# Kernel tuning notes

Hardware: AMD Instinct MI355X
Metric: run time of the kernel (lower is better)

The kernel has to match this reference:

```python
import jax, jax.numpy as jnp
import numpy as np

B, T, C = 4, 1024, 512      # batch, seq_len, n_attn
H, TT, D = 1, 1024, 16      # n_head (forced to 1 by kv.view), ctx_len, head_size


def setup_inputs() -> dict:
    key = jax.random.key(0)
    ks = jax.random.split(key, 13)
    s = 0.02
    return {
        "x": jax.random.normal(ks[0], (B, T, C), jnp.float32),
        "time_w": 1.0 + 0.1 * jax.random.normal(ks[1], (H, TT), jnp.float32),
        "time_alpha": 1.0 + 0.1 * jax.random.normal(ks[2], (H, 1, TT), jnp.float32),
        "time_beta": 1.0 + 0.1 * jax.random.normal(ks[3], (H, TT, 1), jnp.float32),
        "time_gamma": 1.0 + 0.1 * jax.random.normal(ks[4], (TT, 1), jnp.float32),
        "Wk": s * jax.random.normal(ks[5], (D, C), jnp.float32),
        "bk": jnp.zeros((D,), jnp.float32),
        "Wv": s * jax.random.normal(ks[6], (D, C), jnp.float32),
        "bv": jnp.zeros((D,), jnp.float32),
        "Wr": s * jax.random.normal(ks[7], (D, C), jnp.float32),
        "br": jnp.zeros((D,), jnp.float32),
        "Wo": s * jax.random.normal(ks[8], (64, D), jnp.float32),
        "bo": jnp.zeros((64,), jnp.float32),
    }


def reference(x, time_w, time_alpha, time_beta, time_gamma,
              Wk, bk, Wv, bv, Wr, br, Wo, bo):
    Tq = x.shape[1]
    # --- Toeplitz decay-matrix build (pad / tile / reshape trick) ---
    w = jnp.pad(time_w, ((0, 0), (0, TT)))                    # [H, 2TT]
    w = jnp.tile(w, (1, TT))[:, :-TT]                         # [H, 2TT*TT - TT]
    w = w.reshape(-1, TT, 2 * TT - 1)[:, :, TT - 1:]          # [H, TT, TT]
    w = w[:, :Tq, :Tq] * time_alpha[:, :, :Tq] * time_beta[:, :Tq, :]  # [H, T, T]
    # --- time shift on first half of channels (ZeroPad2d((0,0,1,-1))) ---
    half = x.shape[-1] // 2
    xs = jnp.pad(x[:, :, :half], ((0, 0), (1, 0), (0, 0)))[:, :-1]   # shift right by 1
    xx = jnp.concatenate([xs, x[:, :, half:]], axis=-1)              # [B, T, C]
    # --- k / v / r projections ---
    k = jnp.exp(jnp.clip(xx @ Wk.T + bk, -60.0, 30.0))        # [B, T, D]
    v = xx @ Wv.T + bv                                        # [B, T, D]
    r = xx @ Wr.T + br                                        # [B, T, D]
    sum_k = jnp.cumsum(k, axis=1)                             # [B, T, D]
    kv = k * v                                                # [B, T, D]
    # torch: kv.view(B,T,1,D).transpose(1,2) -> [B,1,T,D]; einsum 'htu,bthd->bhud'
    # broadcasts w's h=1 against kv's time axis and kv's t=1 against w's t axis:
    #   wkv[b,h,u,d] = (sum_t w[0,t,u]) * kv[b,h(time),d]
    w_sum = jnp.sum(w, axis=1)[0]                             # [T] over u
    wkv_full = w_sum[None, None, :, None] * kv[:, :, None, :] # [B, T, T, D]
    wkv = jnp.mean(wkv_full, axis=1)                          # mean over h -> [B, T, D]
    rwkv = r * wkv / (sum_k + 1e-8)                           # [B, T, D]
    out = (rwkv @ Wo.T + bo) * time_gamma[:Tq, :]             # [B, T, 64]
    return out
```

## Files before the change

kernel.cpp:

```cpp
#include <hip/hip_runtime.h>
#include <hip/hip_bf16.h>

typedef __hip_bfloat16 bf16;


__device__ __forceinline__ float ldf(const void* p, int f, long idx) {
    if (f == 0) return ((const float*)p)[idx];
    if (f == 1) {
        unsigned int u = ((unsigned int)((const unsigned short*)p)[idx]) << 16;
        float r; __builtin_memcpy(&r, &u, 4); return r;
    }
    return 0.f;
}

__device__ __forceinline__ float4 ld4(const void* p, int f, long idx) {
    if (f == 0) return ((const float4*)p)[idx >> 2];
    if (f == 1) {
        const unsigned short* sp = (const unsigned short*)p + idx;
        unsigned int u0 = ((unsigned int)sp[0]) << 16;
        unsigned int u1 = ((unsigned int)sp[1]) << 16;
        unsigned int u2 = ((unsigned int)sp[2]) << 16;
        unsigned int u3 = ((unsigned int)sp[3]) << 16;
        float4 r;
        __builtin_memcpy(&r.x, &u0, 4); __builtin_memcpy(&r.y, &u1, 4);
        __builtin_memcpy(&r.z, &u2, 4); __builtin_memcpy(&r.w, &u3, 4);
        return r;
    }
    return make_float4(0.f, 0.f, 0.f, 0.f);
}

__device__ __forceinline__ void sniff13(const void* const* ps, const int* ns,
                                        int tid, unsigned* mall, int* sf) {
    unsigned m = 0;
    for (int t = tid; t < 13 * 64; t += 256) {
        int p = t >> 6, j = t & 63;
        int n16 = ns[p] < 64 ? ns[p] : 64;
        if (j < n16) {
            unsigned short v = ((const unsigned short*)ps[p])[j];
            if (v != 0) m |= (1u << p);
        }
    }
    for (int t = tid; t < 13 * 32; t += 256) {
        int p = t >> 5, jp = t & 31;
        int n16 = ns[p] < 64 ? ns[p] : 64; int npair = n16 >> 1;
        if (jp < npair) {
            const unsigned short* u = (const unsigned short*)ps[p];
            unsigned short lo = u[2 * jp], hi = u[2 * jp + 1];
            int elo = (lo >> 7) & 0xFF, ehi = (hi >> 7) & 0xFF;
            bool lo_ok = (elo >= 64 && elo <= 190) || lo == 0;
            bool hi_ok = (ehi >= 64 && ehi <= 190) || hi == 0;
            if (!(lo_ok && hi_ok)) m |= (1u << (16 + p));
        }
    }
    #pragma unroll
    for (int off = 1; off < 64; off <<= 1) m |= __shfl_xor(m, off);
    if (tid == 0) *mall = 0;
    __syncthreads();
    if ((tid & 63) == 0) atomicOr(mall, m);
    __syncthreads();
    unsigned mm = *mall;
    if (tid < 13) {
        int f;
        if (!((mm >> tid) & 1)) f = 2;
        else f = ((mm >> (16 + tid)) & 1) ? 0 : 1;
        sf[tid] = f;
    }
    __syncthreads();
}

__device__ __forceinline__ float ldbias(const void* bk, const void* bv,
                                        const void* br, const int* sf, int o2) {
    if (o2 < 16) return ldf(bk, sf[6], o2);
    if (o2 < 32) return ldf(bv, sf[8], o2 - 16);
    if (o2 < 48) return ldf(br, sf[10], o2 - 32);
    return 0.f;
}

__global__ __launch_bounds__(256) void proj_kernel(
    const void* x, const void* tw, const void* alpha, const void* beta,
    const void* gamma, const void* Wk, const void* bk, const void* Wv,
    const void* bv, const void* Wr, const void* br, const void* Wo,
    const void* bo,
    int n0, int n1, int n2, int n3, int n4, int n5, int n6, int n7,
    int n8, int n9, int n10, int n11, int n12,
    float* __restrict__ k_ws, float* __restrict__ r_ws,
    float* __restrict__ blkS, float* __restrict__ blkKV,
    float* __restrict__ w_sum, int* __restrict__ flags)
{
    __shared__ float xs[8 * 512];
    __shared__ float sred[8][48];
    __shared__ float kred[128], kvred[128];
    __shared__ float wsred[4];
    __shared__ int sf[16];
    __shared__ unsigned mall;
    int tid = threadIdx.x;
    const void* ps[13] = {x,tw,alpha,beta,gamma,Wk,bk,Wv,bv,Wr,br,Wo,bo};
    int ns[13] = {n0,n1,n2,n3,n4,n5,n6,n7,n8,n9,n10,n11,n12};
    sniff13(ps, ns, tid, &mall, sf);

    if (blockIdx.x == 0 && tid < 14) {
        if (tid == 13) {
            int any16 = 0;
            for (int j = 0; j < 13; ++j) if (sf[j] == 1) any16 = 1;
            flags[13] = any16;
        } else {
            flags[tid] = sf[tid];
        }
    }

    int row0 = blockIdx.x * 8;
    int b = row0 >> 10;
    int lt0 = row0 & 1023;
    int fx = sf[0];

    if (fx == 1) {
        const unsigned short* xp = (const unsigned short*)x;
        #pragma unroll
        for (int j = 0; j < 4; ++j) {
            int v = tid + 256 * j;
            int el = v * 4;
            int r = el >> 9, c = el & 511;
            int lt = lt0 + r - ((c < 256) ? 1 : 0);
            float4 f;
            if (lt < 0) f = make_float4(0.f, 0.f, 0.f, 0.f);
            else {
                const unsigned short* sp = xp + ((long)(b * 1024 + lt) * 512 + c);
                unsigned int u0 = ((unsigned int)sp[0]) << 16;
                unsigned int u1 = ((unsigned int)sp[1]) << 16;
                unsigned int u2 = ((unsigned int)sp[2]) << 16;
                unsigned int u3 = ((unsigned int)sp[3]) << 16;
                __builtin_memcpy(&f.x, &u0, 4); __builtin_memcpy(&f.y, &u1, 4);
                __builtin_memcpy(&f.z, &u2, 4); __builtin_memcpy(&f.w, &u3, 4);
            }
            reinterpret_cast<float4*>(xs)[v] = f;
        }
    } else {
        const float* xp = (const float*)x;
        #pragma unroll
        for (int j = 0; j < 4; ++j) {
            int v = tid + 256 * j;
            int el = v * 4;
            int r = el >> 9, c = el & 511;
            int lt = lt0 + r - ((c < 256) ? 1 : 0);
            float4 f;
            if (lt < 0) f = make_float4(0.f, 0.f, 0.f, 0.f);
            else f = *reinterpret_cast<const float4*>(xp + ((long)(b * 1024 + lt) * 512 + c));
            reinterpret_cast<float4*>(xs)[v] = f;
        }
    }
    __syncthreads();

    int lane = tid & 63, wv = tid >> 6;
    const float4* xs4 = reinterpret_cast<const float4*>(xs);
    const void* Wm[3] = {Wk, Wv, Wr};
    int fwm[3] = {sf[5], sf[7], sf[9]};
    #pragma unroll
    for (int m = 0; m < 3; ++m) {
        const void* Wp = Wm[m]; int fw = fwm[m];
        float acc[4][8];
        #pragma unroll
        for (int oi = 0; oi < 4; ++oi)
            #pragma unroll
            for (int r = 0; r < 8; ++r) acc[oi][r] = 0.f;

        if (fw == 0) {
            const float4* Wq = reinterpret_cast<const float4*>(Wp);
            #pragma unroll
            for (int j = 0; j < 2; ++j) {
                int c4 = lane + 64 * j;
                float4 xr[8];
                #pragma unroll
                for (int r = 0; r < 8; ++r) xr[r] = xs4[r * 128 + c4];
                #pragma unroll
                for (int oi = 0; oi < 4; ++oi) {
                    int row = wv * 4 + oi;
                    float4 wq = Wq[row * 128 + c4];
                    #pragma unroll
                    for (int r = 0; r < 8; ++r)
                        acc[oi][r] += xr[r].x * wq.x + xr[r].y * wq.y +
                                      xr[r].z * wq.z + xr[r].w * wq.w;
                }
            }
        } else {
            #pragma unroll
            for (int j = 0; j < 2; ++j) {
                int c4 = lane + 64 * j;
                float4 xr[8];
                #pragma unroll
                for (int r = 0; r < 8; ++r) xr[r] = xs4[r * 128 + c4];
                #pragma unroll
                for (int oi = 0; oi < 4; ++oi) {
                    int row = wv * 4 + oi;
                    float4 wq = ld4(Wp, fw, (long)row * 512 + c4 * 4);
                    #pragma unroll
                    for (int r = 0; r < 8; ++r)
                        acc[oi][r] += xr[r].x * wq.x + xr[r].y * wq.y +
                                      xr[r].z * wq.z + xr[r].w * wq.w;
                }
            }
        }
        #pragma unroll
        for (int oi = 0; oi < 4; ++oi) {
            #pragma unroll
            for (int r = 0; r < 8; ++r) {
                float a = acc[oi][r];
                a += __shfl_xor(a, 1);  a += __shfl_xor(a, 2);
                a += __shfl_xor(a, 4);  a += __shfl_xor(a, 8);
                a += __shfl_xor(a, 16); a += __shfl_xor(a, 32);
                if (lane == oi * 8 + r)
                    sred[r][m * 16 + wv * 4 + oi] = a;
            }
        }
    }
    __syncthreads();

    #pragma unroll
    for (int it = 0; it < 2; ++it) {
        int idx = tid + 256 * it;
        int o2 = idx & 63, r2 = idx >> 6;
        if (o2 < 48) {
            float s = ldbias(bk, bv, br, sf, o2) + sred[r2][o2];
            long a = (long)(lt0 + r2) * 64 + b * 16 + (o2 & 15);
            if (o2 < 16) {
                k_ws[a] = expf(fminf(fmaxf(s, -60.f), 30.f));
            } else if (o2 < 32) {
                int d = o2 - 16;
                float sk = ldbias(bk, bv, br, sf, d) + sred[r2][d];
                float kk = expf(fminf(fmaxf(sk, -60.f), 30.f));
                kred[d * 8 + r2] = kk;
                kvred[d * 8 + r2] = kk * s;
            } else {
                r_ws[a] = s;
            }
        }
    }
    __syncthreads();
    if (tid < 16) {
        float sk = 0.f, skv = 0.f;
        #pragma unroll
        for (int r = 0; r < 8; ++r) { sk += kred[tid * 8 + r]; skv += kvred[tid * 8 + r]; }
        blkS[(long)blockIdx.x * 16 + tid] = sk;
        blkKV[(long)blockIdx.x * 16 + tid] = skv;
    }

    {
        int g = tid >> 7, l = tid & 127;
        int u = blockIdx.x * 2 + g;
        int n = 1024 - u;
        int ftw = sf[1], fbe = sf[3];
        float acc = 0.f;
        for (int s = l; s < n; s += 128)
            acc += ldf(tw, ftw, 1023 - s) * ldf(beta, fbe, u + s);
        #pragma unroll
        for (int off = 32; off > 0; off >>= 1) acc += __shfl_xor(acc, off);
        if ((tid & 63) == 0) wsred[tid >> 6] = acc;
        __syncthreads();
        if ((tid & 127) == 0)
            w_sum[u] = (wsred[g * 2] + wsred[g * 2 + 1]) * ldf(alpha, sf[2], u);
    }
}

__global__ __launch_bounds__(256) void out_kernel(
    const void* gamma, const void* Wo, const void* bo,
    const float* __restrict__ k_ws, const float* __restrict__ r_ws,
    const float* __restrict__ blkS, const float* __restrict__ blkKV,
    const float* __restrict__ w_sum, const int* __restrict__ flags,
    void* __restrict__ out)
{
    __shared__ float redc[256], redk[256];
    __shared__ float cums[16], kvm[16], kk8[8][16], rr8[8][16], rw[8][16];
    __shared__ int sfl[16];
    int tid = threadIdx.x;
    if (tid < 16) sfl[tid] = flags[tid];

    int row0 = blockIdx.x * 8;
    int b = row0 >> 10;
    int t0 = row0 & 1023;
    int nch = t0 >> 3;
    long base = (long)b * 16;

    {
        int d = tid & 15, lane = tid >> 4;
        float pc = 0.f, pk = 0.f;
        for (int ch = lane; ch < nch; ch += 16) pc += blkS[((long)b * 128 + ch) * 16 + d];
        for (int ch = lane; ch < 128; ch += 16) pk += blkKV[((long)b * 128 + ch) * 16 + d];
        redc[tid] = pc; redk[tid] = pk;
    }
    if (tid < 128) {
        int rl = tid >> 4, dd = tid & 15;
        kk8[rl][dd] = k_ws[(long)(t0 + rl) * 64 + base + dd];
    } else {
        int tt = tid - 128; int rl = tt >> 4, dd = tt & 15;
        rr8[rl][dd] = r_ws[(long)(t0 + rl) * 64 + base + dd];
    }
    __syncthreads();
    if (tid < 16) {
        float c = 0.f, kv = 0.f;
        #pragma unroll
        for (int ln = 0; ln < 16; ++ln) { c += redc[ln * 16 + tid]; kv += redk[ln * 16 + tid]; }
        cums[tid] = c;
        kvm[tid] = kv * (1.0f / 1024.0f);
    }
    __syncthreads();

    if (tid < 128) {
        int rl = tid >> 4, o = tid & 15;
        float ck = cums[o];
        for (int i = 0; i <= rl; ++i) ck += kk8[i][o];
        rw[rl][o] = rr8[rl][o] * w_sum[t0 + rl] * kvm[o] / (ck + 1e-8f);
    }
    __syncthreads();

    int fWo = sfl[11], fbo = sfl[12], fga = sfl[4], any16 = sfl[13];
    if (fWo == 0) {
        const float4* Wq = reinterpret_cast<const float4*>(Wo);
        #pragma unroll
        for (int it = 0; it < 2; ++it) {
            int idx = tid + 256 * it;
            int rl = idx >> 6, o = idx & 63;
            int t = t0 + rl;
            float acc = ldf(bo, fbo, o);
            #pragma unroll
            for (int j = 0; j < 4; ++j) {
                float4 w = Wq[o * 4 + j];
                acc += rw[rl][4 * j + 0] * w.x + rw[rl][4 * j + 1] * w.y +
                       rw[rl][4 * j + 2] * w.z + rw[rl][4 * j + 3] * w.w;
            }
            float val = acc * ldf(gamma, fga, t);
            long oa = (long)(row0 + rl) * 64 + o;
            if (any16) ((bf16*)out)[oa] = __float2bfloat16(val);
            else       ((float*)out)[oa] = val;
        }
    } else {
        #pragma unroll
        for (int it = 0; it < 2; ++it) {
            int idx = tid + 256 * it;
            int rl = idx >> 6, o = idx & 63;
            int t = t0 + rl;
            float acc = ldf(bo, fbo, o);
            #pragma unroll
            for (int j = 0; j < 4; ++j) {
                float4 w = ld4(Wo, fWo, (long)o * 16 + 4 * j);
                acc += rw[rl][4 * j + 0] * w.x + rw[rl][4 * j + 1] * w.y +
                       rw[rl][4 * j + 2] * w.z + rw[rl][4 * j + 3] * w.w;
            }
            float val = acc * ldf(gamma, fga, t);
            long oa = (long)(row0 + rl) * 64 + o;
            if (any16) ((bf16*)out)[oa] = __float2bfloat16(val);
            else       ((float*)out)[oa] = val;
        }
    }
}

extern "C" void kernel_launch(void* const* d_in, const int* in_sizes, int n_in,
                              void* d_out, int out_size, void* d_ws, size_t ws_size,
                              hipStream_t stream) {
    const void* x     = d_in[0];
    const void* tw    = d_in[1];
    const void* alpha = d_in[2];
    const void* beta  = d_in[3];
    const void* gamma = d_in[4];
    const void* Wk    = d_in[5];
    const void* bk    = d_in[6];
    const void* Wv    = d_in[7];
    const void* bv    = d_in[8];
    const void* Wr    = d_in[9];
    const void* br    = d_in[10];
    const void* Wo    = d_in[11];
    const void* bo    = d_in[12];

    float* ws    = (float*)d_ws;
    float* k_ws  = ws;
    float* r_ws  = ws + 65536;
    float* blkS  = ws + 131072;
    float* blkKV = ws + 139264;
    float* w_sum = ws + 147456;
    int*   flags = (int*)(ws + 148480);

    proj_kernel<<<512, 256, 0, stream>>>(
        x, tw, alpha, beta, gamma, Wk, bk, Wv, bv, Wr, br, Wo, bo,
        in_sizes[0], in_sizes[1], in_sizes[2], in_sizes[3], in_sizes[4],
        in_sizes[5], in_sizes[6], in_sizes[7], in_sizes[8], in_sizes[9],
        in_sizes[10], in_sizes[11], in_sizes[12],
        k_ws, r_ws, blkS, blkKV, w_sum, flags);
    out_kernel<<<512, 256, 0, stream>>>(
        gamma, Wo, bo, k_ws, r_ws, blkS, blkKV, w_sum, flags, (void*)d_out);
}
```

Before: 115.2 us.

## Fuse projection and output kernels into one persistent kernel with grid barriers

Replaces the two-kernel pipeline with a single 1024-block kernel that uses software grid barriers: one to zero the segment accumulators and build w_sum, and one after the k/v/r projections. Per-block partial sums become atomicAdds into per-64-row segment buffers, which shortens the prefix scan in the output phase. This removes a kernel launch and the second pass over block partials, but depends on all 1024 blocks being co-resident (launch_bounds 256,4), adds a memset, and adds spin-wait costs.

Result: slower. 167.7 us (+45.6%).

```diff
diff --git a/kernel.cpp b/kernel.cpp
--- a/kernel.cpp
+++ b/kernel.cpp
@@ -29,6 +29,13 @@
     return make_float4(0.f, 0.f, 0.f, 0.f);
 }
 
+__device__ __forceinline__ void stc(float* p, float v) {
+    __hip_atomic_store(p, v, __ATOMIC_RELAXED, __HIP_MEMORY_SCOPE_AGENT);
+}
+__device__ __forceinline__ float ldc(const float* p) {
+    return __hip_atomic_load(p, __ATOMIC_RELAXED, __HIP_MEMORY_SCOPE_AGENT);
+}
+
 __device__ __forceinline__ void sniff13(const void* const* ps, const int* ns,
                                         int tid, unsigned* mall, int* sf) {
     unsigned m = 0;
@@ -68,15 +75,20 @@
     __syncthreads();
 }
 
-__device__ __forceinline__ float ldbias(const void* bk, const void* bv,
-                                        const void* br, const int* sf, int o2) {
-    if (o2 < 16) return ldf(bk, sf[6], o2);
-    if (o2 < 32) return ldf(bv, sf[8], o2 - 16);
-    if (o2 < 48) return ldf(br, sf[10], o2 - 32);
-    return 0.f;
-}
-
-__global__ __launch_bounds__(256) void proj_kernel(
+__device__ __forceinline__ void gridbar(unsigned* cnt, unsigned target, int tid) {
+    asm volatile("s_waitcnt vmcnt(0)" ::: "memory");
+    __syncthreads();
+    if (tid == 0) {
+        __hip_atomic_fetch_add(cnt, 1u, __ATOMIC_RELAXED, __HIP_MEMORY_SCOPE_AGENT);
+        while (__hip_atomic_load(cnt, __ATOMIC_RELAXED, __HIP_MEMORY_SCOPE_AGENT)
+               < target)
+            __builtin_amdgcn_s_sleep(4);
+    }
+    __syncthreads();
+    asm volatile("" ::: "memory");
+}
+
+__global__ __launch_bounds__(256, 4) void fused_kernel(
     const void* x, const void* tw, const void* alpha, const void* beta,
     const void* gamma, const void* Wk, const void* bk, const void* Wv,
     const void* bv, const void* Wr, const void* br, const void* Wo,
@@ -84,39 +96,56 @@
     int n0, int n1, int n2, int n3, int n4, int n5, int n6, int n7,
     int n8, int n9, int n10, int n11, int n12,
     float* __restrict__ k_ws, float* __restrict__ r_ws,
-    float* __restrict__ blkS, float* __restrict__ blkKV,
-    float* __restrict__ w_sum, int* __restrict__ flags)
+    float* __restrict__ w_sum, float* __restrict__ segsum,
+    float* __restrict__ segkv, unsigned* __restrict__ cnt,
+    void* __restrict__ out)
 {
-    __shared__ float xs[8 * 512];
-    __shared__ float sred[8][48];
-    __shared__ float kred[128], kvred[128];
-    __shared__ float wsred[4];
+    __shared__ float xs[4 * 512];
+    __shared__ float sred[4][48];
+    __shared__ float kred[64], kvred[64];
+    __shared__ float redc[256], redk[256];
+    __shared__ float cums[16], kvm[16], kk3[3][16], rr4[4][16], rw[4][16], wsl[4];
     __shared__ int sf[16];
     __shared__ unsigned mall;
     int tid = threadIdx.x;
     const void* ps[13] = {x,tw,alpha,beta,gamma,Wk,bk,Wv,bv,Wr,br,Wo,bo};
     int ns[13] = {n0,n1,n2,n3,n4,n5,n6,n7,n8,n9,n10,n11,n12};
+
     sniff13(ps, ns, tid, &mall, sf);
-
-    if (blockIdx.x == 0 && tid < 14) {
-        if (tid == 13) {
-            int any16 = 0;
-            for (int j = 0; j < 13; ++j) if (sf[j] == 1) any16 = 1;
-            flags[13] = any16;
-        } else {
-            flags[tid] = sf[tid];
-        }
-    }
-
-    int row0 = blockIdx.x * 8;
+    if (tid == 0) {
+        int any16 = 0;
+        for (int j = 0; j < 13; ++j) if (sf[j] == 1) any16 = 1;
+        sf[13] = any16;
+    }
+
+    int idx = blockIdx.x * 256 + tid;
+    if (idx < 1024)       stc(&segsum[idx], 0.f);
+    else if (idx < 2048)  stc(&segkv[idx - 1024], 0.f);
+
+    {
+        int u = blockIdx.x;
+        int ftw = sf[1], fal = sf[2], fbe = sf[3];
+        float acc = 0.f;
+        int n = 1024 - u;
+        for (int s = tid; s < n; s += 256)
+            acc += ldf(tw, ftw, 1023 - s) * ldf(beta, fbe, u + s);
+        redc[tid] = acc;
+        __syncthreads();
+        for (int off = 128; off > 0; off >>= 1) {
+            if (tid < off) redc[tid] += redc[tid + off];
+            __syncthreads();
+        }
+        if (tid == 0) stc(&w_sum[u], redc[0] * ldf(alpha, fal, u));
+    }
+
+    int row0 = blockIdx.x * 4;
     int b = row0 >> 10;
     int lt0 = row0 & 1023;
     int fx = sf[0];
-
     if (fx == 1) {
         const unsigned short* xp = (const unsigned short*)x;
         #pragma unroll
-        for (int j = 0; j < 4; ++j) {
+        for (int j = 0; j < 2; ++j) {
             int v = tid + 256 * j;
             int el = v * 4;
             int r = el >> 9, c = el & 511;
@@ -137,7 +166,7 @@
     } else {
         const float* xp = (const float*)x;
         #pragma unroll
-        for (int j = 0; j < 4; ++j) {
+        for (int j = 0; j < 2; ++j) {
             int v = tid + 256 * j;
             int el = v * 4;
             int r = el >> 9, c = el & 511;
@@ -148,207 +177,175 @@
             reinterpret_cast<float4*>(xs)[v] = f;
         }
     }
-    __syncthreads();
-
-    int lane = tid & 63, wv = tid >> 6;
-    const float4* xs4 = reinterpret_cast<const float4*>(xs);
-    const void* Wm[3] = {Wk, Wv, Wr};
-    int fwm[3] = {sf[5], sf[7], sf[9]};
-    #pragma unroll
-    for (int m = 0; m < 3; ++m) {
-        const void* Wp = Wm[m]; int fw = fwm[m];
-        float acc[4][8];
+
+    gridbar(cnt, 1024u, tid);
+
+    {
+        int lane = tid & 63, wv = tid >> 6;
+        const float4* xs4 = reinterpret_cast<const float4*>(xs);
+        const void* Wm[3] = {Wk, Wv, Wr};
+        int fwm[3] = {sf[5], sf[7], sf[9]};
         #pragma unroll
-        for (int oi = 0; oi < 4; ++oi)
-            #pragma unroll
-            for (int r = 0; r < 8; ++r) acc[oi][r] = 0.f;
-
-        if (fw == 0) {
-            const float4* Wq = reinterpret_cast<const float4*>(Wp);
-            #pragma unroll
-            for (int j = 0; j < 2; ++j) {
-                int c4 = lane + 64 * j;
-                float4 xr[8];
+        for (int m = 0; m < 3; ++m) {
+            const void* Wp = Wm[m]; int fw = fwm[m];
+            float acc[4][4];
+            #pragma unroll
+            for (int oi = 0; oi < 4; ++oi)
                 #pragma unroll
-                for (int r = 0; r < 8; ++r) xr[r] = xs4[r * 128 + c4];
+                for (int r = 0; r < 4; ++r) acc[oi][r] = 0.f;
+
+            if (fw == 0) {
+                const float4* Wq = reinterpret_cast<const float4*>(Wp);
                 #pragma unroll
-                for (int oi = 0; oi < 4; ++oi) {
-                    int row = wv * 4 + oi;
-                    float4 wq = Wq[row * 128 + c4];
+                for (int j = 0; j < 2; ++j) {
+                    int c4 = lane + 64 * j;
+                    float4 xr[4];
                     #pragma unroll
-                    for (int r = 0; r < 8; ++r)
-                        acc[oi][r] += xr[r].x * wq.x + xr[r].y * wq.y +
-                                      xr[r].z * wq.z + xr[r].w * wq.w;
+                    for (int r = 0; r < 4; ++r) xr[r] = xs4[r * 128 + c4];
+                    #pragma unroll
+                    for (int oi = 0; oi < 4; ++oi) {
+                        int row = wv * 4 + oi;
+                        float4 wq = Wq[row * 128 + c4];
+                        #pragma unroll
+                        for (int r = 0; r < 4; ++r)
+                            acc[oi][r] += xr[r].x * wq.x + xr[r].y * wq.y +
+                                          xr[r].z * wq.z + xr[r].w * wq.w;
+                    }
                 }
-            }
-        } else {
-            #pragma unroll
-            for (int j = 0; j < 2; ++j) {
-                int c4 = lane + 64 * j;
-                float4 xr[8];
+            } else {
                 #pragma unroll
-                for (int r = 0; r < 8; ++r) xr[r] = xs4[r * 128 + c4];
+                for (int j = 0; j < 2; ++j) {
+                    int c4 = lane + 64 * j;
+                    float4 xr[4];
+                    #pragma unroll
+                    for (int r = 0; r < 4; ++r) xr[r] = xs4[r * 128 + c4];
+                    #pragma unroll
+                    for (int oi = 0; oi < 4; ++oi) {
+                        int row = wv * 4 + oi;
+                        float4 wq = ld4(Wp, fw, (long)row * 512 + c4 * 4);
+                        #pragma unroll
+                        for (int r = 0; r < 4; ++r)
+                            acc[oi][r] += xr[r].x * wq.x + xr[r].y * wq.y +
+                                          xr[r].z * wq.z + xr[r].w * wq.w;
+                    }
+                }
+            }
+            #pragma unroll
+            for (int oi = 0; oi < 4; ++oi) {
                 #pragma unroll
-                for (int oi = 0; oi < 4; ++oi) {
-                    int row = wv * 4 + oi;
-                    float4 wq = ld4(Wp, fw, (long)row * 512 + c4 * 4);
-                    #pragma unroll
-                    for (int r = 0; r < 8; ++r)
-                        acc[oi][r] += xr[r].x * wq.x + xr[r].y * wq.y +
-                                      xr[r].z * wq.z + xr[r].w * wq.w;
+                for (int r = 0; r < 4; ++r) {
+                    float a = acc[oi][r];
+                    a += __shfl_xor(a, 1);  a += __shfl_xor(a, 2);
+                    a += __shfl_xor(a, 4);  a += __shfl_xor(a, 8);
+                    a += __shfl_xor(a, 16); a += __shfl_xor(a, 32);
+                    if (lane == oi * 4 + r)
+                        sred[r][m * 16 + wv * 4 + oi] = a;
                 }
             }
         }
-        #pragma unroll
-        for (int oi = 0; oi < 4; ++oi) {
-            #pragma unroll
-            for (int r = 0; r < 8; ++r) {
-                float a = acc[oi][r];
-                a += __shfl_xor(a, 1);  a += __shfl_xor(a, 2);
-                a += __shfl_xor(a, 4);  a += __shfl_xor(a, 8);
-                a += __shfl_xor(a, 16); a += __shfl_xor(a, 32);
-                if (lane == oi * 8 + r)
-                    sred[r][m * 16 + wv * 4 + oi] = a;
-            }
-        }
-    }
-    __syncthreads();
-
-    #pragma unroll
-    for (int it = 0; it < 2; ++it) {
-        int idx = tid + 256 * it;
-        int o2 = idx & 63, r2 = idx >> 6;
+        __syncthreads();
+
+        int o2 = tid & 63, r2 = tid >> 6;
+        int seg = lt0 >> 6;
         if (o2 < 48) {
-            float s = ldbias(bk, bv, br, sf, o2) + sred[r2][o2];
+            float s = 0.f;
+            if (o2 < 16)      s = ldf(bk, sf[6], o2);
+            else if (o2 < 32) s = ldf(bv, sf[8], o2 - 16);
+            else              s = ldf(br, sf[10], o2 - 32);
+            s += sred[r2][o2];
             long a = (long)(lt0 + r2) * 64 + b * 16 + (o2 & 15);
             if (o2 < 16) {
-                k_ws[a] = expf(fminf(fmaxf(s, -60.f), 30.f));
+                stc(&k_ws[a], expf(fminf(fmaxf(s, -60.f), 30.f)));
             } else if (o2 < 32) {
                 int d = o2 - 16;
-                float sk = ldbias(bk, bv, br, sf, d) + sred[r2][d];
+                float sk = ldf(bk, sf[6], d) + sred[r2][d];
                 float kk = expf(fminf(fmaxf(sk, -60.f), 30.f));
-                kred[d * 8 + r2] = kk;
-                kvred[d * 8 + r2] = kk * s;
+                kred[d * 4 + r2] = kk;
+                kvred[d * 4 + r2] = kk * s;
             } else {
-                r_ws[a] = s;
-            }
-        }
-    }
-    __syncthreads();
-    if (tid < 16) {
-        float sk = 0.f, skv = 0.f;
-        #pragma unroll
-        for (int r = 0; r < 8; ++r) { sk += kred[tid * 8 + r]; skv += kvred[tid * 8 + r]; }
-        blkS[(long)blockIdx.x * 16 + tid] = sk;
-        blkKV[(long)blockIdx.x * 16 + tid] = skv;
-    }
+                stc(&r_ws[a], s);
+            }
+        }
+        __syncthreads();
+        if (tid < 16) {
+            float sk = 0.f, skv = 0.f;
+            #pragma unroll
+            for (int r = 0; r < 4; ++r) { sk += kred[tid * 4 + r]; skv += kvred[tid * 4 + r]; }
+            atomicAdd(&segsum[seg * 64 + b * 16 + tid], sk);
+            atomicAdd(&segkv[seg * 64 + b * 16 + tid], skv);
+        }
+    }
+
+    gridbar(cnt, 2048u, tid);
 
     {
-        int g = tid >> 7, l = tid & 127;
-        int u = blockIdx.x * 2 + g;
-        int n = 1024 - u;
-        int ftw = sf[1], fbe = sf[3];
-        float acc = 0.f;
-        for (int s = l; s < n; s += 128)
-            acc += ldf(tw, ftw, 1023 - s) * ldf(beta, fbe, u + s);
-        #pragma unroll
-        for (int off = 32; off > 0; off >>= 1) acc += __shfl_xor(acc, off);
-        if ((tid & 63) == 0) wsred[tid >> 6] = acc;
-        __syncthreads();
-        if ((tid & 127) == 0)
-            w_sum[u] = (wsred[g * 2] + wsred[g * 2 + 1]) * ldf(alpha, sf[2], u);
-    }
-}
-
-__global__ __launch_bounds__(256) void out_kernel(
-    const void* gamma, const void* Wo, const void* bo,
-    const float* __restrict__ k_ws, const float* __restrict__ r_ws,
-    const float* __restrict__ blkS, const float* __restrict__ blkKV,
-    const float* __restrict__ w_sum, const int* __restrict__ flags,
-    void* __restrict__ out)
-{
-    __shared__ float redc[256], redk[256];
-    __shared__ float cums[16], kvm[16], kk8[8][16], rr8[8][16], rw[8][16];
-    __shared__ int sfl[16];
-    int tid = threadIdx.x;
-    if (tid < 16) sfl[tid] = flags[tid];
-
-    int row0 = blockIdx.x * 8;
-    int b = row0 >> 10;
-    int t0 = row0 & 1023;
-    int nch = t0 >> 3;
-    long base = (long)b * 16;
-
-    {
-        int d = tid & 15, lane = tid >> 4;
-        float pc = 0.f, pk = 0.f;
-        for (int ch = lane; ch < nch; ch += 16) pc += blkS[((long)b * 128 + ch) * 16 + d];
-        for (int ch = lane; ch < 128; ch += 16) pk += blkKV[((long)b * 128 + ch) * 16 + d];
-        redc[tid] = pc; redk[tid] = pk;
-    }
-    if (tid < 128) {
-        int rl = tid >> 4, dd = tid & 15;
-        kk8[rl][dd] = k_ws[(long)(t0 + rl) * 64 + base + dd];
-    } else {
-        int tt = tid - 128; int rl = tt >> 4, dd = tt & 15;
-        rr8[rl][dd] = r_ws[(long)(t0 + rl) * 64 + base + dd];
-    }
-    __syncthreads();
-    if (tid < 16) {
-        float c = 0.f, kv = 0.f;
-        #pragma unroll
-        for (int ln = 0; ln < 16; ++ln) { c += redc[ln * 16 + tid]; kv += redk[ln * 16 + tid]; }
-        cums[tid] = c;
-        kvm[tid] = kv * (1.0f / 1024.0f);
-    }
-    __syncthreads();
-
-    if (tid < 128) {
-        int rl = tid >> 4, o = tid & 15;
-        float ck = cums[o];
-        for (int i = 0; i <= rl; ++i) ck += kk8[i][o];
-        rw[rl][o] = rr8[rl][o] * w_sum[t0 + rl] * kvm[o] / (ck + 1e-8f);
-    }
-    __syncthreads();
-
-    int fWo = sfl[11], fbo = sfl[12], fga = sfl[4], any16 = sfl[13];
-    if (fWo == 0) {
-        const float4* Wq = reinterpret_cast<const float4*>(Wo);
-        #pragma unroll
-        for (int it = 0; it < 2; ++it) {
-            int idx = tid + 256 * it;
-            int rl = idx >> 6, o = idx & 63;
-            int t = t0 + rl;
-            float acc = ldf(bo, fbo, o);
+        int t0 = lt0;
+        int seg = t0 >> 6;
+        int ncum = ((t0 + 3) & 63) + 1;
+        long base = (long)b * 16;
+
+        int d = tid & 15, ln = tid >> 4;
+        float pc = 0.f;
+        for (int i = ln; i < ncum; i += 16)
+            pc += ldc(&k_ws[(long)(seg * 64 + i) * 64 + base + d]);
+        for (int s2 = ln; s2 < seg; s2 += 16)
+            pc += ldc(&segsum[s2 * 64 + base + d]);
+        redc[tid] = pc;
+        redk[tid] = ldc(&segkv[ln * 64 + base + d]);
+        __syncthreads();
+
+        if (tid < 16) {
+            float c = 0.f, kv = 0.f;
+            #pragma unroll
+            for (int l2 = 0; l2 < 16; ++l2) { c += redc[l2 * 16 + tid]; kv += redk[l2 * 16 + tid]; }
+            cums[tid] = c;
+            kvm[tid] = kv * (1.0f / 1024.0f);
+        } else if (tid < 64) {
+            int rr = (tid >> 4) - 1;
+            int dd = tid & 15;
+            kk3[rr][dd] = ldc(&k_ws[(long)(t0 + 1 + rr) * 64 + base + dd]);
+        } else if (tid < 128) {
+            int tt = tid - 64; int rl = tt >> 4, dd = tt & 15;
+            rr4[rl][dd] = ldc(&r_ws[(long)(t0 + rl) * 64 + base + dd]);
+        } else if (tid < 132) {
+            wsl[tid - 128] = ldc(&w_sum[t0 + tid - 128]);
+        }
+        __syncthreads();
+
+        if (tid < 64) {
+            int rl = tid >> 4, o = tid & 15;
+            float ck = cums[o];
+            #pragma unroll
+            for (int j = 2; j >= 0; --j)
+                if (rl <= j) ck -= kk3[j][o];
+            rw[rl][o] = rr4[rl][o] * wsl[rl] * kvm[o] / (ck + 1e-8f);
+        }
+        __syncthreads();
+
+        int fWo = sf[11], fbo = sf[12], fga = sf[4], any16 = sf[13];
+        int rl = tid >> 6, o = tid & 63;
+        int t = t0 + rl;
+        float acc = ldf(bo, fbo, o);
+        if (fWo == 0) {
+            const float4* Wq = reinterpret_cast<const float4*>(Wo);
             #pragma unroll
             for (int j = 0; j < 4; ++j) {
                 float4 w = Wq[o * 4 + j];
                 acc += rw[rl][4 * j + 0] * w.x + rw[rl][4 * j + 1] * w.y +
                        rw[rl][4 * j + 2] * w.z + rw[rl][4 * j + 3] * w.w;
             }
-            float val = acc * ldf(gamma, fga, t);
-            long oa = (long)(row0 + rl) * 64 + o;
-            if (any16) ((bf16*)out)[oa] = __float2bfloat16(val);
-            else       ((float*)out)[oa] = val;
-        }
-    } else {
-        #pragma unroll
-        for (int it = 0; it < 2; ++it) {
-            int idx = tid + 256 * it;
-            int rl = idx >> 6, o = idx & 63;
-            int t = t0 + rl;
-            float acc = ldf(bo, fbo, o);
+        } else {
             #pragma unroll
             for (int j = 0; j < 4; ++j) {
                 float4 w = ld4(Wo, fWo, (long)o * 16 + 4 * j);
                 acc += rw[rl][4 * j + 0] * w.x + rw[rl][4 * j + 1] * w.y +
                        rw[rl][4 * j + 2] * w.z + rw[rl][4 * j + 3] * w.w;
             }
-            float val = acc * ldf(gamma, fga, t);
-            long oa = (long)(row0 + rl) * 64 + o;
-            if (any16) ((bf16*)out)[oa] = __float2bfloat16(val);
-            else       ((float*)out)[oa] = val;
-        }
+        }
+        float val = acc * ldf(gamma, fga, t);
+        long oa = (long)(row0 + rl) * 64 + o;
+        if (any16) ((bf16*)out)[oa] = __float2bfloat16(val);
+        else       ((float*)out)[oa] = val;
     }
 }
 
@@ -369,20 +366,19 @@
     const void* Wo    = d_in[11];
     const void* bo    = d_in[12];
 
-    float* ws    = (float*)d_ws;
-    float* k_ws  = ws;
-    float* r_ws  = ws + 65536;
-    float* blkS  = ws + 131072;
-    float* blkKV = ws + 139264;
-    float* w_sum = ws + 147456;
-    int*   flags = (int*)(ws + 148480);
-
-    proj_kernel<<<512, 256, 0, stream>>>(
+    float* ws     = (float*)d_ws;
+    float* k_ws   = ws;
+    float* r_ws   = ws + 65536;
+    float* w_sum  = ws + 131072;
+    float* segsum = ws + 132096;
+    float* segkv  = ws + 133120;
+    unsigned* cnt = (unsigned*)(ws + 134144);
+
+    hipMemsetAsync((void*)cnt, 0, sizeof(unsigned), stream);
+    fused_kernel<<<1024, 256, 0, stream>>>(
         x, tw, alpha, beta, gamma, Wk, bk, Wv, bv, Wr, br, Wo, bo,
         in_sizes[0], in_sizes[1], in_sizes[2], in_sizes[3], in_sizes[4],
         in_sizes[5], in_sizes[6], in_sizes[7], in_sizes[8], in_sizes[9],
         in_sizes[10], in_sizes[11], in_sizes[12],
-        k_ws, r_ws, blkS, blkKV, w_sum, flags);
-    out_kernel<<<512, 256, 0, stream>>>(
-        gamma, Wo, bo, k_ws, r_ws, blkS, blkKV, w_sum, flags, (void*)d_out);
-}
+        k_ws, r_ws, w_sum, segsum, segkv, cnt, (void*)d_out);
+}
```

## Fuse projection and output kernels into one persistent kernel with grid barriers

Applied to the files above, without the earlier changes.

Merges the two launches into a single 512-block kernel that uses a hierarchical atomic grid barrier (32-block groups plus a super counter) to order the phases. Per-block partial sums are replaced by atomically accumulated 64-row segment sums, and the prefix sum over k now reads a transposed k layout within the current segment. This is meant to remove the second launch and the inter-kernel gap. In exchange it adds a memset launch and spin-wait barriers, which deadlock unless all 512 blocks are co-resident; launch_bounds(256,2) is set to help with that.

After: 126.8 us. 10.1% more time.

```diff
diff --git a/kernel.cpp b/kernel.cpp
--- a/kernel.cpp
+++ b/kernel.cpp
@@ -29,6 +29,13 @@
     return make_float4(0.f, 0.f, 0.f, 0.f);
 }
 
+__device__ __forceinline__ void stc(float* p, float v) {
+    __hip_atomic_store(p, v, __ATOMIC_RELAXED, __HIP_MEMORY_SCOPE_AGENT);
+}
+__device__ __forceinline__ float ldc(const float* p) {
+    return __hip_atomic_load(p, __ATOMIC_RELAXED, __HIP_MEMORY_SCOPE_AGENT);
+}
+
 __device__ __forceinline__ void sniff13(const void* const* ps, const int* ns,
                                         int tid, unsigned* mall, int* sf) {
     unsigned m = 0;
@@ -68,15 +75,28 @@
     __syncthreads();
 }
 
-__device__ __forceinline__ float ldbias(const void* bk, const void* bv,
-                                        const void* br, const int* sf, int o2) {
-    if (o2 < 16) return ldf(bk, sf[6], o2);
-    if (o2 < 32) return ldf(bv, sf[8], o2 - 16);
-    if (o2 < 48) return ldf(br, sf[10], o2 - 32);
-    return 0.f;
-}
-
-__global__ __launch_bounds__(256) void proj_kernel(
+__device__ __forceinline__ void gridbar(unsigned* barr, int phase,
+                                        int bid, int tid) {
+    asm volatile("s_waitcnt vmcnt(0)" ::: "memory");
+    __syncthreads();
+    if (tid == 0) {
+        unsigned* g = &barr[(bid >> 5) * 16];
+        unsigned* super = &barr[256];
+        unsigned old = __hip_atomic_fetch_add(g, 1u, __ATOMIC_RELAXED,
+                                              __HIP_MEMORY_SCOPE_AGENT);
+        if (old == (unsigned)(phase * 32 - 1))
+            __hip_atomic_fetch_add(super, 1u, __ATOMIC_RELAXED,
+                                   __HIP_MEMORY_SCOPE_AGENT);
+        while (__hip_atomic_load(super, __ATOMIC_RELAXED,
+                                 __HIP_MEMORY_SCOPE_AGENT)
+               < (unsigned)(phase * 16))
+            __builtin_amdgcn_s_sleep(8);
+    }
+    __syncthreads();
+    asm volatile("" ::: "memory");
+}
+
+__global__ __launch_bounds__(256, 2) void fused_kernel(
     const void* x, const void* tw, const void* alpha, const void* beta,
     const void* gamma, const void* Wk, const void* bk, const void* Wv,
     const void* bv, const void* Wr, const void* br, const void* Wo,
@@ -84,35 +104,37 @@
     int n0, int n1, int n2, int n3, int n4, int n5, int n6, int n7,
     int n8, int n9, int n10, int n11, int n12,
     float* __restrict__ k_ws, float* __restrict__ r_ws,
-    float* __restrict__ blkS, float* __restrict__ blkKV,
-    float* __restrict__ w_sum, int* __restrict__ flags)
+    float* __restrict__ w_sum, float* __restrict__ segsum,
+    float* __restrict__ segkv, unsigned* __restrict__ barr,
+    void* __restrict__ out)
 {
     __shared__ float xs[8 * 512];
-    __shared__ float sred[8][48];
-    __shared__ float kred[128], kvred[128];
-    __shared__ float wsred[4];
+    __shared__ float sred[3 * 8 * 16];
+    __shared__ float kred[128], kvred[128], wsred[4];
+    __shared__ float redc[256], redk[256];
+    __shared__ float cums[16], kvm[16], kk8[8][16], rr8[8][16], rw[8][16], wsl[8];
     __shared__ int sf[16];
     __shared__ unsigned mall;
     int tid = threadIdx.x;
+    int bid = blockIdx.x;
     const void* ps[13] = {x,tw,alpha,beta,gamma,Wk,bk,Wv,bv,Wr,br,Wo,bo};
     int ns[13] = {n0,n1,n2,n3,n4,n5,n6,n7,n8,n9,n10,n11,n12};
+
     sniff13(ps, ns, tid, &mall, sf);
-
-    if (blockIdx.x == 0 && tid < 14) {
-        if (tid == 13) {
-            int any16 = 0;
-            for (int j = 0; j < 13; ++j) if (sf[j] == 1) any16 = 1;
-            flags[13] = any16;
-        } else {
-            flags[tid] = sf[tid];
-        }
-    }
-
-    int row0 = blockIdx.x * 8;
+    if (tid == 0) {
+        int any16 = 0;
+        for (int j = 0; j < 13; ++j) if (sf[j] == 1) any16 = 1;
+        sf[13] = any16;
+    }
+
+    int zidx = bid * 256 + tid;
+    if (zidx < 1024)       stc(&segsum[zidx], 0.f);
+    else if (zidx < 2048)  stc(&segkv[zidx - 1024], 0.f);
+
+    int row0 = bid * 8;
     int b = row0 >> 10;
     int lt0 = row0 & 1023;
     int fx = sf[0];
-
     if (fx == 1) {
         const unsigned short* xp = (const unsigned short*)x;
         #pragma unroll
@@ -148,104 +170,10 @@
             reinterpret_cast<float4*>(xs)[v] = f;
         }
     }
-    __syncthreads();
-
-    int lane = tid & 63, wv = tid >> 6;
-    const float4* xs4 = reinterpret_cast<const float4*>(xs);
-    const void* Wm[3] = {Wk, Wv, Wr};
-    int fwm[3] = {sf[5], sf[7], sf[9]};
-    #pragma unroll
-    for (int m = 0; m < 3; ++m) {
-        const void* Wp = Wm[m]; int fw = fwm[m];
-        float acc[4][8];
-        #pragma unroll
-        for (int oi = 0; oi < 4; ++oi)
-            #pragma unroll
-            for (int r = 0; r < 8; ++r) acc[oi][r] = 0.f;
-
-        if (fw == 0) {
-            const float4* Wq = reinterpret_cast<const float4*>(Wp);
-            #pragma unroll
-            for (int j = 0; j < 2; ++j) {
-                int c4 = lane + 64 * j;
-                float4 xr[8];
-                #pragma unroll
-                for (int r = 0; r < 8; ++r) xr[r] = xs4[r * 128 + c4];
-                #pragma unroll
-                for (int oi = 0; oi < 4; ++oi) {
-                    int row = wv * 4 + oi;
-                    float4 wq = Wq[row * 128 + c4];
-                    #pragma unroll
-                    for (int r = 0; r < 8; ++r)
-                        acc[oi][r] += xr[r].x * wq.x + xr[r].y * wq.y +
-                                      xr[r].z * wq.z + xr[r].w * wq.w;
-                }
-            }
-        } else {
-            #pragma unroll
-            for (int j = 0; j < 2; ++j) {
-                int c4 = lane + 64 * j;
-                float4 xr[8];
-                #pragma unroll
-                for (int r = 0; r < 8; ++r) xr[r] = xs4[r * 128 + c4];
-                #pragma unroll
-                for (int oi = 0; oi < 4; ++oi) {
-                    int row = wv * 4 + oi;
-                    float4 wq = ld4(Wp, fw, (long)row * 512 + c4 * 4);
-                    #pragma unroll
-                    for (int r = 0; r < 8; ++r)
-                        acc[oi][r] += xr[r].x * wq.x + xr[r].y * wq.y +
-                                      xr[r].z * wq.z + xr[r].w * wq.w;
-                }
-            }
-        }
-        #pragma unroll
-        for (int oi = 0; oi < 4; ++oi) {
-            #pragma unroll
-            for (int r = 0; r < 8; ++r) {
-                float a = acc[oi][r];
-                a += __shfl_xor(a, 1);  a += __shfl_xor(a, 2);
-                a += __shfl_xor(a, 4);  a += __shfl_xor(a, 8);
-                a += __shfl_xor(a, 16); a += __shfl_xor(a, 32);
-                if (lane == oi * 8 + r)
-                    sred[r][m * 16 + wv * 4 + oi] = a;
-            }
-        }
-    }
-    __syncthreads();
-
-    #pragma unroll
-    for (int it = 0; it < 2; ++it) {
-        int idx = tid + 256 * it;
-        int o2 = idx & 63, r2 = idx >> 6;
-        if (o2 < 48) {
-            float s = ldbias(bk, bv, br, sf, o2) + sred[r2][o2];
-            long a = (long)(lt0 + r2) * 64 + b * 16 + (o2 & 15);
-            if (o2 < 16) {
-                k_ws[a] = expf(fminf(fmaxf(s, -60.f), 30.f));
-            } else if (o2 < 32) {
-                int d = o2 - 16;
-                float sk = ldbias(bk, bv, br, sf, d) + sred[r2][d];
-                float kk = expf(fminf(fmaxf(sk, -60.f), 30.f));
-                kred[d * 8 + r2] = kk;
-                kvred[d * 8 + r2] = kk * s;
-            } else {
-                r_ws[a] = s;
-            }
-        }
-    }
-    __syncthreads();
-    if (tid < 16) {
-        float sk = 0.f, skv = 0.f;
-        #pragma unroll
-        for (int r = 0; r < 8; ++r) { sk += kred[tid * 8 + r]; skv += kvred[tid * 8 + r]; }
-        blkS[(long)blockIdx.x * 16 + tid] = sk;
-        blkKV[(long)blockIdx.x * 16 + tid] = skv;
-    }
 
     {
         int g = tid >> 7, l = tid & 127;
-        int u = blockIdx.x * 2 + g;
+        int u = bid * 2 + g;
         int n = 1024 - u;
         int ftw = sf[1], fbe = sf[3];
         float acc = 0.f;
@@ -256,93 +184,182 @@
         if ((tid & 63) == 0) wsred[tid >> 6] = acc;
         __syncthreads();
         if ((tid & 127) == 0)
-            w_sum[u] = (wsred[g * 2] + wsred[g * 2 + 1]) * ldf(alpha, sf[2], u);
-    }
-}
-
-__global__ __launch_bounds__(256) void out_kernel(
-    const void* gamma, const void* Wo, const void* bo,
-    const float* __restrict__ k_ws, const float* __restrict__ r_ws,
-    const float* __restrict__ blkS, const float* __restrict__ blkKV,
-    const float* __restrict__ w_sum, const int* __restrict__ flags,
-    void* __restrict__ out)
-{
-    __shared__ float redc[256], redk[256];
-    __shared__ float cums[16], kvm[16], kk8[8][16], rr8[8][16], rw[8][16];
-    __shared__ int sfl[16];
-    int tid = threadIdx.x;
-    if (tid < 16) sfl[tid] = flags[tid];
-
-    int row0 = blockIdx.x * 8;
-    int b = row0 >> 10;
-    int t0 = row0 & 1023;
-    int nch = t0 >> 3;
-    long base = (long)b * 16;
+            stc(&w_sum[u], (wsred[g * 2] + wsred[g * 2 + 1]) * ldf(alpha, sf[2], u));
+    }
+
+    gridbar(barr, 1, bid, tid);
 
     {
-        int d = tid & 15, lane = tid >> 4;
-        float pc = 0.f, pk = 0.f;
-        for (int ch = lane; ch < nch; ch += 16) pc += blkS[((long)b * 128 + ch) * 16 + d];
-        for (int ch = lane; ch < 128; ch += 16) pk += blkKV[((long)b * 128 + ch) * 16 + d];
-        redc[tid] = pc; redk[tid] = pk;
-    }
-    if (tid < 128) {
-        int rl = tid >> 4, dd = tid & 15;
-        kk8[rl][dd] = k_ws[(long)(t0 + rl) * 64 + base + dd];
-    } else {
-        int tt = tid - 128; int rl = tt >> 4, dd = tt & 15;
-        rr8[rl][dd] = r_ws[(long)(t0 + rl) * 64 + base + dd];
-    }
-    __syncthreads();
-    if (tid < 16) {
-        float c = 0.f, kv = 0.f;
-        #pragma unroll
-        for (int ln = 0; ln < 16; ++ln) { c += redc[ln * 16 + tid]; kv += redk[ln * 16 + tid]; }
-        cums[tid] = c;
-        kvm[tid] = kv * (1.0f / 1024.0f);
-    }
-    __syncthreads();
-
-    if (tid < 128) {
-        int rl = tid >> 4, o = tid & 15;
-        float ck = cums[o];
-        for (int i = 0; i <= rl; ++i) ck += kk8[i][o];
-        rw[rl][o] = rr8[rl][o] * w_sum[t0 + rl] * kvm[o] / (ck + 1e-8f);
-    }
-    __syncthreads();
-
-    int fWo = sfl[11], fbo = sfl[12], fga = sfl[4], any16 = sfl[13];
-    if (fWo == 0) {
-        const float4* Wq = reinterpret_cast<const float4*>(Wo);
+        int lane = tid & 63, wv = tid >> 6;
+        const float4* xs4 = reinterpret_cast<const float4*>(xs);
+        const void* Wm[3] = {Wk, Wv, Wr};
+        int fwm[3] = {sf[5], sf[7], sf[9]};
+        #pragma unroll
+        for (int m = 0; m < 3; ++m) {
+            const void* Wp = Wm[m]; int fw = fwm[m];
+            float acc[4][8];
+            #pragma unroll
+            for (int oi = 0; oi < 4; ++oi)
+                #pragma unroll
+                for (int r = 0; r < 8; ++r) acc[oi][r] = 0.f;
+
+            if (fw == 0) {
+                const float4* Wq = reinterpret_cast<const float4*>(Wp);
+                #pragma unroll
+                for (int j = 0; j < 2; ++j) {
+                    int c4 = lane + 64 * j;
+                    float4 xr[8];
+                    #pragma unroll
+                    for (int r = 0; r < 8; ++r) xr[r] = xs4[r * 128 + c4];
+                    #pragma unroll
+                    for (int oi = 0; oi < 4; ++oi) {
+                        int row = wv * 4 + oi;
+                        float4 wq = Wq[row * 128 + c4];
+                        #pragma unroll
+                        for (int r = 0; r < 8; ++r)
+                            acc[oi][r] += xr[r].x * wq.x + xr[r].y * wq.y +
+                                          xr[r].z * wq.z + xr[r].w * wq.w;
+                    }
+                }
+            } else {
+                #pragma unroll
+                for (int j = 0; j < 2; ++j) {
+                    int c4 = lane + 64 * j;
+                    float4 xr[8];
+                    #pragma unroll
+                    for (int r = 0; r < 8; ++r) xr[r] = xs4[r * 128 + c4];
+                    #pragma unroll
+                    for (int oi = 0; oi < 4; ++oi) {
+                        int row = wv * 4 + oi;
+                        float4 wq = ld4(Wp, fw, (long)row * 512 + c4 * 4);
+                        #pragma unroll
+                        for (int r = 0; r < 8; ++r)
+                            acc[oi][r] += xr[r].x * wq.x + xr[r].y * wq.y +
+                                          xr[r].z * wq.z + xr[r].w * wq.w;
+                    }
+                }
+            }
+            #pragma unroll
+            for (int oi = 0; oi < 4; ++oi) {
+                #pragma unroll
+                for (int r = 0; r < 8; ++r) {
+                    float a = acc[oi][r];
+                    a += __shfl_xor(a, 1);  a += __shfl_xor(a, 2);
+                    a += __shfl_xor(a, 4);  a += __shfl_xor(a, 8);
+                    a += __shfl_xor(a, 16); a += __shfl_xor(a, 32);
+                    if (lane == oi * 8 + r)
+                        sred[(m * 8 + r) * 16 + wv * 4 + oi] = a;
+                }
+            }
+        }
+        __syncthreads();
+
+        int seg = lt0 >> 6;
+        #pragma unroll
+        for (int it = 0; it < 2; ++it) {
+            int idx = tid + 256 * it;
+            int o2 = idx & 63, r2 = idx >> 6;
+            if (o2 < 48) {
+                int m = o2 >> 4, oo = o2 & 15;
+                float s = 0.f;
+                if (o2 < 16)      s = ldf(bk, sf[6], o2);
+                else if (o2 < 32) s = ldf(bv, sf[8], o2 - 16);
+                else              s = ldf(br, sf[10], o2 - 32);
+                s += sred[(m * 8 + r2) * 16 + oo];
+                if (o2 < 16) {
+                    stc(&k_ws[(long)(b * 16 + o2) * 1024 + lt0 + r2],
+                        expf(fminf(fmaxf(s, -60.f), 30.f)));
+                } else if (o2 < 32) {
+                    int d = o2 - 16;
+                    float sk = ldf(bk, sf[6], d) + sred[(0 * 8 + r2) * 16 + d];
+                    float kk = expf(fminf(fmaxf(sk, -60.f), 30.f));
+                    kred[d * 8 + r2] = kk;
+                    kvred[d * 8 + r2] = kk * s;
+                } else {
+                    stc(&r_ws[(long)(lt0 + r2) * 64 + b * 16 + (o2 & 15)], s);
+                }
+            }
+        }
+        __syncthreads();
+        if (tid < 16) {
+            float sk = 0.f, skv = 0.f;
+            #pragma unroll
+            for (int r = 0; r < 8; ++r) { sk += kred[tid * 8 + r]; skv += kvred[tid * 8 + r]; }
+            atomicAdd(&segsum[(b * 16 + tid) * 16 + seg], sk);
+            atomicAdd(&segkv[(b * 16 + tid) * 16 + seg], skv);
+        }
+    }
+
+    gridbar(barr, 2, bid, tid);
+
+    {
+        int t0 = lt0;
+        int seg = t0 >> 6;
+        int ncum = ((t0 + 7) & 63) + 1;
+        int rel0 = t0 & 63;
+        int base16 = b * 16;
+
+        int d = tid >> 4, i0 = tid & 15;
+        const float* kcol = k_ws + (long)(base16 + d) * 1024;
+        float pc = 0.f;
+        for (int i = i0; i < ncum; i += 16) {
+            float v = ldc(&kcol[seg * 64 + i]);
+            pc += v;
+            int rel = i - rel0;
+            if ((unsigned)rel < 8u) kk8[rel][d] = v;
+        }
+        for (int s2 = i0; s2 < seg; s2 += 16)
+            pc += ldc(&segsum[(base16 + d) * 16 + s2]);
+        redc[tid] = pc;
+        redk[tid] = ldc(&segkv[(base16 + d) * 16 + i0]);
+        __syncthreads();
+
+        if (tid < 16) {
+            float c = 0.f, kv = 0.f;
+            #pragma unroll
+            for (int q = 0; q < 16; ++q) { c += redc[tid * 16 + q]; kv += redk[tid * 16 + q]; }
+            cums[tid] = c;
+            kvm[tid] = kv * (1.0f / 1024.0f);
+        } else if (tid < 24) {
+            wsl[tid - 16] = ldc(&w_sum[t0 + tid - 16]);
+        } else if (tid >= 128) {
+            int idx = tid - 128; int rl = idx >> 4, dd = idx & 15;
+            rr8[rl][dd] = ldc(&r_ws[(long)(t0 + rl) * 64 + base16 + dd]);
+        }
+        __syncthreads();
+
+        if (tid < 128) {
+            int rl = tid >> 4, o = tid & 15;
+            float ck = cums[o];
+            #pragma unroll
+            for (int i = 1; i < 8; ++i)
+                if (i > rl) ck -= kk8[i][o];
+            rw[rl][o] = rr8[rl][o] * wsl[rl] * kvm[o] / (ck + 1e-8f);
+        }
+        __syncthreads();
+
+        int fWo = sf[11], fbo = sf[12], fga = sf[4], any16 = sf[13];
         #pragma unroll
         for (int it = 0; it < 2; ++it) {
             int idx = tid + 256 * it;
             int rl = idx >> 6, o = idx & 63;
             int t = t0 + rl;
             float acc = ldf(bo, fbo, o);
-            #pragma unroll
-            for (int j = 0; j < 4; ++j) {
-                float4 w = Wq[o * 4 + j];
-                acc += rw[rl][4 * j + 0] * w.x + rw[rl][4 * j + 1] * w.y +
-                       rw[rl][4 * j + 2] * w.z + rw[rl][4 * j + 3] * w.w;
-            }
-            float val = acc * ldf(gamma, fga, t);
-            long oa = (long)(row0 + rl) * 64 + o;
-            if (any16) ((bf16*)out)[oa] = __float2bfloat16(val);
-            else       ((float*)out)[oa] = val;
-        }
-    } else {
-        #pragma unroll
-        for (int it = 0; it < 2; ++it) {
-            int idx = tid + 256 * it;
-            int rl = idx >> 6, o = idx & 63;
-            int t = t0 + rl;
-            float acc = ldf(bo, fbo, o);
-            #pragma unroll
-            for (int j = 0; j < 4; ++j) {
-                float4 w = ld4(Wo, fWo, (long)o * 16 + 4 * j);
-                acc += rw[rl][4 * j + 0] * w.x + rw[rl][4 * j + 1] * w.y +
-                       rw[rl][4 * j + 2] * w.z + rw[rl][4 * j + 3] * w.w;
+            if (fWo == 0) {
+                const float4* Wq = reinterpret_cast<const float4*>(Wo);
+                #pragma unroll
+                for (int j = 0; j < 4; ++j) {
+                    float4 w = Wq[o * 4 + j];
+                    acc += rw[rl][4 * j + 0] * w.x + rw[rl][4 * j + 1] * w.y +
+                           rw[rl][4 * j + 2] * w.z + rw[rl][4 * j + 3] * w.w;
+                }
+            } else {
+                #pragma unroll
+                for (int j = 0; j < 4; ++j) {
+                    float4 w = ld4(Wo, fWo, (long)o * 16 + 4 * j);
+                    acc += rw[rl][4 * j + 0] * w.x + rw[rl][4 * j + 1] * w.y +
+                           rw[rl][4 * j + 2] * w.z + rw[rl][4 * j + 3] * w.w;
+                }
             }
             float val = acc * ldf(gamma, fga, t);
             long oa = (long)(row0 + rl) * 64 + o;
@@ -369,20 +386,19 @@
     const void* Wo    = d_in[11];
     const void* bo    = d_in[12];
 
-    float* ws    = (float*)d_ws;
-    float* k_ws  = ws;
-    float* r_ws  = ws + 65536;
-    float* blkS  = ws + 131072;
-    float* blkKV = ws + 139264;
-    float* w_sum = ws + 147456;
-    int*   flags = (int*)(ws + 148480);
-
-    proj_kernel<<<512, 256, 0, stream>>>(
+    float* ws     = (float*)d_ws;
+    float* k_ws   = ws;
+    float* r_ws   = ws + 65536;
+    float* w_sum  = ws + 131072;
+    float* segsum = ws + 132096;
+    float* segkv  = ws + 133120;
+    unsigned* barr = (unsigned*)(ws + 134144);
+
+    hipMemsetAsync((void*)barr, 0, 272 * sizeof(unsigned), stream);
+    fused_kernel<<<512, 256, 0, stream>>>(
         x, tw, alpha, beta, gamma, Wk, bk, Wv, bv, Wr, br, Wo, bo,
         in_sizes[0], in_sizes[1], in_sizes[2], in_sizes[3], in_sizes[4],
         in_sizes[5], in_sizes[6], in_sizes[7], in_sizes[8], in_sizes[9],
         in_sizes[10], in_sizes[11], in_sizes[12],
-        k_ws, r_ws, blkS, blkKV, w_sum, flags);
-    out_kernel<<<512, 256, 0, stream>>>(
-        gamma, Wo, bo, k_ws, r_ws, blkS, blkKV, w_sum, flags, (void*)d_out);
-}
+        k_ws, r_ws, w_sum, segsum, segkv, barr, (void*)d_out);
+}
```
